# Kernel optimization log

Measured on AMD Instinct MI355X. Metric: run time of the kernel, lower is better.

## Reference

```python
import jax, jax.numpy as jnp
import numpy as np
from jax import lax

HIDDEN = 7168
Q_LORA = 1536
N_HEAD = 64
HEAD_DIM = 128
ROPE_DIM = 64
TOPK = 2048
T = 4096
ROPE_BASE = 10000.0
LN_EPS = 1e-6
NEG_INF = -1e30


def _apply_rope_interleaved(x, cos, sin):
    # x: [..., ROPE_DIM], cos/sin broadcastable to [..., ROPE_DIM//2]
    x1 = x[..., 0::2]
    x2 = x[..., 1::2]
    o1 = x1 * cos - x2 * sin
    o2 = x1 * sin + x2 * cos
    out = jnp.stack([o1, o2], axis=-1)  # interleave back
    return out.reshape(x.shape)


def setup_inputs() -> dict:
    key = jax.random.key(0)
    ks = jax.random.split(key, 6)
    hidden_states = jax.random.normal(ks[0], (T, HIDDEN), dtype=jnp.float32)
    qr = jax.random.normal(ks[1], (T, Q_LORA), dtype=jnp.float32)
    positions = jnp.arange(T, dtype=jnp.int32)
    # learned parameters (stored [in, out] so fwd is x @ W)
    Wq_b = jax.random.normal(ks[2], (Q_LORA, N_HEAD * HEAD_DIM), dtype=jnp.float32) * 0.02
    Wk = jax.random.normal(ks[3], (HIDDEN, HEAD_DIM), dtype=jnp.float32) * 0.02
    Wproj = jax.random.normal(ks[4], (HIDDEN, N_HEAD), dtype=jnp.float32) * 0.02
    k_norm_gamma = jnp.ones((HEAD_DIM,), dtype=jnp.float32)
    k_norm_beta = jnp.zeros((HEAD_DIM,), dtype=jnp.float32)
    return {
        'hidden_states': hidden_states,
        'qr': qr,
        'positions': positions,
        'Wq_b': Wq_b,
        'Wk': Wk,
        'Wproj': Wproj,
        'k_norm_gamma': k_norm_gamma,
        'k_norm_beta': k_norm_beta,
    }


def _indexer_forward(hidden_states, qr, positions, Wq_b, Wk, Wproj, gamma, beta):
    # q projection: [T, n_head * head_dim] -> [T, H, D]
    q = (qr @ Wq_b).reshape(T, N_HEAD, HEAD_DIM)
    q_pe, q_nope = q[..., :ROPE_DIM], q[..., ROPE_DIM:]

    # k projection + LayerNorm (eps=1e-6)
    k = hidden_states @ Wk  # [T, D]
    mu = jnp.mean(k, axis=-1, keepdims=True)
    var = jnp.mean(jnp.square(k - mu), axis=-1, keepdims=True)
    k = (k - mu) * lax.rsqrt(var + LN_EPS) * gamma + beta
    k_pe, k_nope = k[..., :ROPE_DIM], k[..., ROPE_DIM:]

    # RoPE (interleaved / GPT-J style, as used by DeepSeek rotary)
    inv_freq = 1.0 / (ROPE_BASE ** (jnp.arange(0, ROPE_DIM, 2, dtype=jnp.float32) / ROPE_DIM))
    ang = positions.astype(jnp.float32)[:, None] * inv_freq[None, :]  # [T, R/2]
    cos, sin = jnp.cos(ang), jnp.sin(ang)
    q_pe = _apply_rope_interleaved(q_pe, cos[:, None, :], sin[:, None, :])  # [T, H, R]
    k_pe = _apply_rope_interleaved(k_pe, cos, sin)  # [T, R]

    q_full = jnp.concatenate([q_pe, q_nope], axis=-1)  # [T, H, D]
    k_full = jnp.concatenate([k_pe, k_nope], axis=-1)  # [T, D]

    # per-token per-head weights, scaled by head_dim**-0.5 * n_head**-0.5
    w = (hidden_states @ Wproj) * (HEAD_DIM ** -0.5) * (N_HEAD ** -0.5)  # [T, H]

    # lightning-indexer score: sum_h w[t,h] * relu(q[t,h,:] . k[s,:])
    # scan over heads so live intermediate is a single [T, T] matrix
    qh_all = jnp.transpose(q_full, (1, 0, 2))  # [H, T, D]
    wh_all = w.T  # [H, T]

    def body(acc, hw):
        qh, wh = hw  # [T, D], [T]
        acc = acc + wh[:, None] * jax.nn.relu(qh @ k_full.T)
        return acc, None

    scores, _ = lax.scan(body, jnp.zeros((T, T), dtype=jnp.float32), (qh_all, wh_all))

    # causal mask over key positions, then select top-k keys per query
    causal = positions[:, None] >= positions[None, :]
    masked = jnp.where(causal, scores, NEG_INF)
    topk_vals, topk_idx = lax.top_k(masked, TOPK)  # [T, TOPK]
    return topk_vals, topk_idx


def reference(hidden_states, qr, positions, Wq_b, Wk, Wproj, k_norm_gamma, k_norm_beta):
    return _indexer_forward(hidden_states, qr, positions, Wq_b, Wk, Wproj, k_norm_gamma, k_norm_beta)
```

## Files before the change

### kernel.cpp

```cpp
#include <hip/hip_runtime.h>
#include <stdint.h>

#define TT 4096
#define HID 7168
#define QL 1536
#define NH 64
#define HD 128
#define QD 8192
#define KTOP 2048
#define WSCALE 0.011048543456039806f

typedef _Float16 f16;
typedef uint16_t u16;
typedef unsigned u32;
typedef __attribute__((ext_vector_type(4))) float f32x4;
typedef __attribute__((ext_vector_type(16))) float f32x16;
typedef __attribute__((ext_vector_type(8))) _Float16 f16x8;
typedef __attribute__((ext_vector_type(4))) _Float16 f16x4;

__device__ __forceinline__ void lds_load16(const void* g, void* l) {
  __builtin_amdgcn_global_load_lds(
      (const __attribute__((address_space(1))) unsigned*)g,
      (__attribute__((address_space(3))) unsigned*)l, 16, 0, 0);
}

__device__ __forceinline__ u16 f16_bits(f16 h) {
  union { f16 h; u16 u; } c; c.h = h; return c.u;
}
__device__ __forceinline__ float f16_from_bits(u16 u) {
  union { u16 u; f16 h; } c; c.u = u; return (float)c.h;
}

__device__ __forceinline__ size_t soff(int t) {
  int b = t >> 7, r = t & 127;
  return (size_t)128u * ((size_t)(b + 1) * (size_t)(64 * b + r));
}

__global__ void tcvt(const float* __restrict__ in, f16* __restrict__ out,
                     int R, int C, int ostride, int orow0) {
  __shared__ float tile[32][33];
  int cb = blockIdx.x * 32, rb = blockIdx.y * 32;
  int tx = threadIdx.x & 31, ty = threadIdx.x >> 5;
  for (int i = 0; i < 32; i += 8)
    tile[ty + i][tx] = in[(size_t)(rb + ty + i) * C + cb + tx];
  __syncthreads();
  for (int i = 0; i < 32; i += 8)
    out[(size_t)(cb + ty + i + orow0) * ostride + rb + tx] = (f16)tile[tx][ty + i];
}

__launch_bounds__(256, 2)
__global__ void gemm_q(const float* __restrict__ A, const f16* __restrict__ B, f16* __restrict__ C) {
  __shared__ __align__(16) f16 As[128 * 32];
  __shared__ __align__(16) f16 Bs[128 * 32];
  int tid = threadIdx.x, lane = tid & 63, wave = tid >> 6;
  int bm = blockIdx.y << 7, bn = blockIdx.x << 7;
  int wm = (wave & 1) << 6, wn = (wave >> 1) << 6;
  const f16* gb = B + (size_t)(bn + (tid >> 2)) * QL + (tid & 3) * 8;
  f16* lB = Bs + wave * 512;
  int ar = tid >> 3, ac = (tid & 7) * 4;
  f32x4 acc[4][4] = {};
  for (int k0 = 0; k0 < QL; k0 += 32) {
    __syncthreads();
#pragma unroll
    for (int i = 0; i < 4; i++) {
      float4 v = *(const float4*)(A + (size_t)(bm + ar + i * 32) * QL + k0 + ac);
      f16x4 h = {(f16)v.x, (f16)v.y, (f16)v.z, (f16)v.w};
      *(f16x4*)(As + (ar + i * 32) * 32 + ac) = h;
    }
    lds_load16(gb + k0, lB);
    lds_load16(gb + (size_t)64 * QL + k0, lB + 2048);
    __syncthreads();
    int ro = lane & 15, ko = (lane >> 4) << 3;
    f16x8 af[4], bf[4];
#pragma unroll
    for (int i = 0; i < 4; i++) af[i] = *(const f16x8*)(As + (wm + i * 16 + ro) * 32 + ko);
#pragma unroll
    for (int i = 0; i < 4; i++) bf[i] = *(const f16x8*)(Bs + (wn + i * 16 + ro) * 32 + ko);
#pragma unroll
    for (int mi = 0; mi < 4; mi++)
#pragma unroll
      for (int ni = 0; ni < 4; ni++)
        acc[mi][ni] = __builtin_amdgcn_mfma_f32_16x16x32_f16(af[mi], bf[ni], acc[mi][ni], 0, 0, 0);
  }
  int cr = (lane >> 4) << 2, cc = lane & 15;
#pragma unroll
  for (int mi = 0; mi < 4; mi++)
#pragma unroll
    for (int ni = 0; ni < 4; ni++) {
      int row = bm + wm + mi * 16 + cr;
      int col = bn + wn + ni * 16 + cc;
      f16* cp = C + (size_t)row * QD + col;
#pragma unroll
      for (int r = 0; r < 4; r++) cp[(size_t)r * QD] = (f16)acc[mi][ni][r];
    }
}

__launch_bounds__(256, 2)
__global__ void gemm_kw(const float* __restrict__ A, const f16* __restrict__ B,
                        float* __restrict__ kraw, float* __restrict__ wout) {
  __shared__ __align__(16) f16 As[64 * 64];
  __shared__ __align__(16) f16 Bs[64 * 64];
  int tid = threadIdx.x, lane = tid & 63, wave = tid >> 6;
  int bm = blockIdx.y << 6, bn = blockIdx.x << 6;
  int wm = (wave & 1) << 5, wn = (wave >> 1) << 5;
  const f16* gb = B + (size_t)(bn + (tid >> 3)) * HID + (tid & 7) * 8;
  f16* lB = Bs + wave * 512;
  int ar = tid >> 4, ac = (tid & 15) * 4;
  f32x4 acc[2][2] = {};
  for (int k0 = 0; k0 < HID; k0 += 64) {
    __syncthreads();
#pragma unroll
    for (int i = 0; i < 4; i++) {
      float4 v = *(const float4*)(A + (size_t)(bm + ar + i * 16) * HID + k0 + ac);
      f16x4 h = {(f16)v.x, (f16)v.y, (f16)v.z, (f16)v.w};
      *(f16x4*)(As + (ar + i * 16) * 64 + ac) = h;
    }
    lds_load16(gb + k0, lB);
    lds_load16(gb + (size_t)32 * HID + k0, lB + 2048);
    __syncthreads();
    int ro = lane & 15, ko = (lane >> 4) << 3;
    f16x8 af[2][2], bf[2][2];
#pragma unroll
    for (int i = 0; i < 2; i++)
#pragma unroll
      for (int kk = 0; kk < 2; kk++) {
        af[i][kk] = *(const f16x8*)(As + (wm + i * 16 + ro) * 64 + kk * 32 + ko);
        bf[i][kk] = *(const f16x8*)(Bs + (wn + i * 16 + ro) * 64 + kk * 32 + ko);
      }
#pragma unroll
    for (int mi = 0; mi < 2; mi++)
#pragma unroll
      for (int ni = 0; ni < 2; ni++)
#pragma unroll
        for (int kk = 0; kk < 2; kk++)
          acc[mi][ni] = __builtin_amdgcn_mfma_f32_16x16x32_f16(af[mi][kk], bf[ni][kk], acc[mi][ni], 0, 0, 0);
  }
  int cr = (lane >> 4) << 2, cc = lane & 15;
#pragma unroll
  for (int mi = 0; mi < 2; mi++)
#pragma unroll
    for (int ni = 0; ni < 2; ni++) {
      int row = bm + wm + mi * 16 + cr;
      int col = bn + wn + ni * 16 + cc;
#pragma unroll
      for (int r = 0; r < 4; r++) {
        float v = acc[mi][ni][r];
        int rr = row + r;
        if (col < HD) kraw[(size_t)rr * HD + col] = v;
        else          wout[(size_t)rr * NH + (col - HD)] = v * WSCALE;
      }
    }
}

__global__ void ln_rope(const float* __restrict__ kraw, const int* __restrict__ pos,
                        const float* __restrict__ gamma, const float* __restrict__ beta,
                        f16* __restrict__ k16) {
  int row = (blockIdx.x << 2) + (threadIdx.x >> 6);
  int lane = threadIdx.x & 63;
  const float* kr = kraw + (size_t)row * HD;
  float2 x = ((const float2*)kr)[lane];
  float s = x.x + x.y, s2 = x.x * x.x + x.y * x.y;
  for (int off = 32; off; off >>= 1) { s += __shfl_down(s, off); s2 += __shfl_down(s2, off); }
  s = __shfl(s, 0); s2 = __shfl(s2, 0);
  float mu = s * (1.f / 128.f);
  float var = s2 * (1.f / 128.f) - mu * mu;
  float inv = rsqrtf(var + 1e-6f);
  float y0 = (x.x - mu) * inv * gamma[lane * 2] + beta[lane * 2];
  float y1 = (x.y - mu) * inv * gamma[lane * 2 + 1] + beta[lane * 2 + 1];
  float o0 = y0, o1 = y1;
  if (lane < 32) {
    float p = (float)pos[row];
    float invf = exp2f(-(float)lane * 0.41524101185942813f);
    float ang = p * invf;
    float sn, cn;
    sincosf(ang, &sn, &cn);
    o0 = y0 * cn - y1 * sn;
    o1 = y0 * sn + y1 * cn;
  }
  k16[(size_t)row * HD + 2 * lane] = (f16)o0;
  k16[(size_t)row * HD + 2 * lane + 1] = (f16)o1;
}

__global__ void rope_q(f16* __restrict__ q16, const int* __restrict__ pos) {
  int t = blockIdx.x, tid = threadIdx.x;
  __shared__ float cs[64];
  if (tid < 32) {
    float invf = exp2f(-(float)tid * 0.41524101185942813f);
    float ang = (float)pos[t] * invf;
    float sn, cn;
    sincosf(ang, &sn, &cn);
    cs[tid] = cn;
    cs[32 + tid] = sn;
  }
  __syncthreads();
  f16* row = q16 + (size_t)t * QD;
#pragma unroll
  for (int it = 0; it < 2; it++) {
    int u = it * 256 + tid;
    int h = u >> 3, c = u & 7;
    f16* p = row + h * HD + c * 8;
    f16x8 v = *(f16x8*)p;
#pragma unroll
    for (int j = 0; j < 4; j++) {
      int l = c * 4 + j;
      float cn = cs[l], sn = cs[32 + l];
      float x = (float)v[2 * j], y = (float)v[2 * j + 1];
      v[2 * j] = (f16)(x * cn - y * sn);
      v[2 * j + 1] = (f16)(x * sn + y * cn);
    }
    *(f16x8*)p = v;
  }
}

__launch_bounds__(256, 3)
__global__ void scores2(const f16* __restrict__ q16, const f16* __restrict__ k16,
                        const float* __restrict__ w, f16* __restrict__ S) {
  int kt0 = blockIdx.x << 8;
  int qt0 = blockIdx.y << 5;
  if (kt0 > qt0 + 31) return;
  int tid = threadIdx.x, l = tid & 63, wid = tid >> 6;
  int q = l & 31, half = l >> 5;
  __shared__ __align__(16) f16 smem_q[8192];
  __shared__ float w_lds[2048];

  for (int i = tid; i < 2048; i += 256) {
    int hh = i & 63, qq = i >> 6;
    w_lds[hh * 32 + qq] = w[(size_t)(qt0 + qq) * NH + hh];
  }
  f16x8 kfr[2][8];
  {
    const f16* kb = k16 + (size_t)(kt0 + wid * 64 + q) * HD + half * 8;
#pragma unroll
    for (int mt = 0; mt < 2; mt++)
#pragma unroll
      for (int kk = 0; kk < 8; kk++)
        kfr[mt][kk] = *(const f16x8*)(kb + mt * 32 * HD + kk * 16);
  }
  const f16* qbase = q16 + (size_t)qt0 * QD;
#pragma unroll
  for (int p = 0; p < 2; p++) {
    int u = p * 256 + tid;
    lds_load16(qbase + (size_t)(u & 31) * QD + (u >> 5) * 8, smem_q + u * 8);
  }
  f32x16 s0 = {}, s1 = {};
  __syncthreads();

  for (int h = 0; h < NH; h++) {
    if (h < NH - 1) {
      const f16* src = qbase + (h + 1) * HD;
      f16* dst = smem_q + ((h + 1) & 1) * 4096;
#pragma unroll
      for (int p = 0; p < 2; p++) {
        int u = p * 256 + tid;
        lds_load16(src + (size_t)(u & 31) * QD + (u >> 5) * 8, dst + u * 8);
      }
    }
    const f16* qb = smem_q + (h & 1) * 4096;
    f32x16 a0 = {}, a1 = {};
#pragma unroll
    for (int kk = 0; kk < 8; kk++) {
      f16x8 qf = *(const f16x8*)(qb + ((kk * 2 + half) * 32 + q) * 8);
      a0 = __builtin_amdgcn_mfma_f32_32x32x16_f16(kfr[0][kk], qf, a0, 0, 0, 0);
      a1 = __builtin_amdgcn_mfma_f32_32x32x16_f16(kfr[1][kk], qf, a1, 0, 0, 0);
    }
    float wv = w_lds[h * 32 + q];
#pragma unroll
    for (int r = 0; r < 16; r++) {
      s0[r] += wv * fmaxf(a0[r], 0.f);
      s1[r] += wv * fmaxf(a1[r], 0.f);
    }
    __syncthreads();
  }

  f16* st = smem_q;
#pragma unroll
  for (int mt = 0; mt < 2; mt++)
#pragma unroll
    for (int r = 0; r < 16; r++) {
      int m = (r & 3) + ((r >> 2) << 3) + half * 4;
      int sl = wid * 64 + mt * 32 + m;
      float v = mt ? s1[r] : s0[r];
      if (!(v == v)) v = 0.f;
      v = fminf(fmaxf(v, -60000.f), 60000.f);
      u32 byte = (u32)(q * 512 + sl * 2) ^ (u32)((q & 7) << 4);
      *(f16*)((char*)st + byte) = (f16)v;
    }
  __syncthreads();
  {
    int rq = tid >> 3, c = tid & 7;
    int t = qt0 + rq;
    size_t base = soff(t) + (size_t)kt0;
    bool hi = (t - kt0) >= 128;
#pragma unroll
    for (int j = 0; j < 4; j++) {
      if (c < 4 || hi) {
        u32 byte = (u32)(rq * 512 + c * 64 + j * 16) ^ (u32)((rq & 7) << 4);
        uint4 v = *(uint4*)((char*)st + byte);
        *(uint4*)(S + base + c * 32 + j * 8) = v;
      }
    }
  }
}

template <int N>
__device__ __forceinline__ void sort_and_store(u32* key, int tid, int t, float* out) {
  constexpr int V = N / 256;
  u32 v[V];
#pragma unroll
  for (int r = 0; r < V; r += 4) {
    uint4 q4 = *(const uint4*)(key + tid * V + r);
    v[r] = ~q4.x; v[r + 1] = ~q4.y; v[r + 2] = ~q4.z; v[r + 3] = ~q4.w;
  }
#pragma unroll
  for (int k = 2; k <= N; k <<= 1) {
#pragma unroll
    for (int j = k >> 1; j > 0; j >>= 1) {
      if (j >= 64 * V) {
#pragma unroll
        for (int r = 0; r < V; r += 4) {
          uint4 q4 = {v[r], v[r + 1], v[r + 2], v[r + 3]};
          *(uint4*)(key + tid * V + r) = q4;
        }
        __syncthreads();
        for (int m = tid; m < N / 2; m += 256) {
          int i = ((m & ~(j - 1)) << 1) | (m & (j - 1));
          int l = i | j;
          bool up = ((i & k) == 0);
          u32 a = key[i], b = key[l];
          if (up ? (a > b) : (a < b)) { key[i] = b; key[l] = a; }
        }
        __syncthreads();
#pragma unroll
        for (int r = 0; r < V; r += 4) {
          uint4 q4 = *(const uint4*)(key + tid * V + r);
          v[r] = q4.x; v[r + 1] = q4.y; v[r + 2] = q4.z; v[r + 3] = q4.w;
        }
      } else if (j >= V) {
        int lanej = j / V;
        bool takeMin = (((tid & lanej) == 0) == (((tid * V) & k) == 0));
#pragma unroll
        for (int r = 0; r < V; r++) {
          u32 o = __shfl_xor(v[r], lanej, 64);
          u32 mn = min(v[r], o), mx = max(v[r], o);
          v[r] = takeMin ? mn : mx;
        }
      } else {
#pragma unroll
        for (int r = 0; r < V; r++) {
          if ((r & j) == 0) {
            bool up = (((tid * V + r) & k) == 0);
            u32 a = v[r], b = v[r | j];
            u32 mn = min(a, b), mx = max(a, b);
            v[r] = up ? mn : mx;
            v[r | j] = up ? mx : mn;
          }
        }
      }
    }
  }
  if (tid * V < KTOP) {
    float* ov = out + (size_t)t * KTOP + tid * V;
    float* oi = out + (size_t)TT * KTOP + (size_t)t * KTOP + tid * V;
#pragma unroll
    for (int r = 0; r < V; r++) {
      u32 kv = ~v[r];
      u32 mono = kv >> 16;
      float val;
      if (mono == 0u) {
        val = -1e30f;
      } else {
        u16 hb = (u16)((mono & 0x8000u) ? (mono ^ 0x8000u) : (mono ^ 0xFFFFu));
        val = f16_from_bits(hb);
      }
      ov[r] = val;
      oi[r] = (float)(0xFFFFu - (kv & 0xFFFFu));
    }
  }
}

__launch_bounds__(256, 4)
__global__ void topk_k(const f16* __restrict__ S, float* __restrict__ out) {
  int t = blockIdx.x, tid = threadIdx.x;
  __shared__ __align__(16) u32 key[4096];
  size_t base = soff(t);
  int nsort = (t <= 2047) ? 2048 : 4096;
  const uint4* src = (const uint4*)(S + base);
  for (int i = tid; i < (nsort >> 3); i += 256) {
    uint4 v4 = src[i];
    u32 ww[4] = {v4.x, v4.y, v4.z, v4.w};
#pragma unroll
    for (int j = 0; j < 8; j++) {
      int s = i * 8 + j;
      u32 kk;
      if (s > t) {
        kk = 0xFFFFu - (u32)s;
      } else {
        u16 hb = (u16)(ww[j >> 1] >> ((j & 1) * 16));
        u32 mono = (hb & 0x8000u) ? (u32)(hb ^ 0xFFFFu) : (u32)(hb | 0x8000u);
        kk = (mono << 16) | (0xFFFFu - (u32)s);
      }
      key[s] = kk;
    }
  }
  __syncthreads();
  if (t <= 2047) sort_and_store<2048>(key, tid, t, out);
  else           sort_and_store<4096>(key, tid, t, out);
}

extern "C" void kernel_launch(void* const* d_in, const int* in_sizes, int n_in,
                              void* d_out, int out_size, void* d_ws, size_t ws_size,
                              hipStream_t stream) {
  const float* hs = (const float*)d_in[0];
  const float* qr = (const float*)d_in[1];
  const int* pos = (const int*)d_in[2];
  const float* Wq = (const float*)d_in[3];
  const float* Wk = (const float*)d_in[4];
  const float* Wp = (const float*)d_in[5];
  const float* gamma = (const float*)d_in[6];
  const float* beta = (const float*)d_in[7];
  char* ws = (char*)d_ws;
  float* kraw = (float*)ws;
  float* wsc = (float*)(ws + 2097152);
  f16* k16 = (f16*)(ws + 3145728);
  f16* kwT = (f16*)(ws + 4194304);
  f16* wqT = (f16*)(ws + 6946816);
  f16* q16 = (f16*)(ws + 32112640);
  f16* S = (f16*)(ws + 4194304);

  tcvt<<<dim3(256, 48), dim3(256), 0, stream>>>(Wq, wqT, QL, QD, QL, 0);
  tcvt<<<dim3(4, 224), dim3(256), 0, stream>>>(Wk, kwT, HID, HD, HID, 0);
  tcvt<<<dim3(2, 224), dim3(256), 0, stream>>>(Wp, kwT, HID, NH, HID, HD);
  gemm_kw<<<dim3(3, 64), dim3(256), 0, stream>>>(hs, kwT, kraw, wsc);
  ln_rope<<<dim3(1024), dim3(256), 0, stream>>>(kraw, pos, gamma, beta, k16);
  gemm_q<<<dim3(64, 32), dim3(256), 0, stream>>>(qr, wqT, q16);
  rope_q<<<dim3(4096), dim3(256), 0, stream>>>(q16, pos);
  scores2<<<dim3(16, 128), dim3(256), 0, stream>>>(q16, k16, wsc, S);
  topk_k<<<dim3(4096), dim3(256), 0, stream>>>(S, (float*)d_out);
}
```

Before: 860.1 us.

## Launch only causal score tiles and deepen Q staging to four-stage pipeline

Replaces the 16x128 grid with early-exit blocks by a compact 1088-block grid that maps each block to a lower-triangular (query, key) tile, interleaved across XCDs. The per-head Q staging in shared memory goes from double to quad buffering, with explicit vmcnt waits and raw barriers so three heads are in flight, and MFMA sections get raised wave priority. This is meant to remove the cost of empty blocks, hide global-to-LDS latency, and cut full __syncthreads overhead. In exchange LDS use doubles, which may lower occupancy, and the hand-written waitcnt counts must match the number of outstanding loads.

```diff
diff --git a/kernel.cpp b/kernel.cpp
--- a/kernel.cpp
+++ b/kernel.cpp
@@ -215,12 +215,18 @@
 __launch_bounds__(256, 3)
 __global__ void scores2(const f16* __restrict__ q16, const f16* __restrict__ k16,
                         const float* __restrict__ w, f16* __restrict__ S) {
-  int kt0 = blockIdx.x << 8;
-  int qt0 = blockIdx.y << 5;
-  if (kt0 > qt0 + 31) return;
+  int bid = (int)blockIdx.x;
+  bid = (bid & 7) * 136 + (bid >> 3);
+  int g = 0;
+  while (4 * (g + 1) * (g + 2) <= bid) g++;
+  int rem = bid - 4 * g * (g + 1);
+  int qt = (g << 3) + rem / (g + 1);
+  int kt = rem - (rem / (g + 1)) * (g + 1);
+  int kt0 = kt << 8, qt0 = qt << 5;
+
   int tid = threadIdx.x, l = tid & 63, wid = tid >> 6;
   int q = l & 31, half = l >> 5;
-  __shared__ __align__(16) f16 smem_q[8192];
+  __shared__ __align__(16) f16 smem_q[4 * 4096];
   __shared__ float w_lds[2048];
 
   for (int i = tid; i < 2048; i += 256) {
@@ -236,41 +242,60 @@
       for (int kk = 0; kk < 8; kk++)
         kfr[mt][kk] = *(const f16x8*)(kb + mt * 32 * HD + kk * 16);
   }
+  __syncthreads();
+  asm volatile("s_waitcnt vmcnt(0)" ::: "memory");
+
   const f16* qbase = q16 + (size_t)qt0 * QD;
-#pragma unroll
-  for (int p = 0; p < 2; p++) {
-    int u = p * 256 + tid;
-    lds_load16(qbase + (size_t)(u & 31) * QD + (u >> 5) * 8, smem_q + u * 8);
-  }
+  auto stage = [&](int h) {
+    const f16* src = qbase + h * HD;
+    f16* dst = smem_q + (h & 3) * 4096;
+#pragma unroll
+    for (int p = 0; p < 2; p++) {
+      int u = p * 256 + tid;
+      lds_load16(src + (size_t)(u & 31) * QD + (u >> 5) * 8, dst + u * 8);
+    }
+  };
+
   f32x16 s0 = {}, s1 = {};
-  __syncthreads();
-
-  for (int h = 0; h < NH; h++) {
-    if (h < NH - 1) {
-      const f16* src = qbase + (h + 1) * HD;
-      f16* dst = smem_q + ((h + 1) & 1) * 4096;
-#pragma unroll
-      for (int p = 0; p < 2; p++) {
-        int u = p * 256 + tid;
-        lds_load16(src + (size_t)(u & 31) * QD + (u >> 5) * 8, dst + u * 8);
-      }
-    }
-    const f16* qb = smem_q + (h & 1) * 4096;
+  auto compute = [&](int h) {
+    const f16* qb = smem_q + (h & 3) * 4096;
     f32x16 a0 = {}, a1 = {};
+    __builtin_amdgcn_s_setprio(1);
 #pragma unroll
     for (int kk = 0; kk < 8; kk++) {
       f16x8 qf = *(const f16x8*)(qb + ((kk * 2 + half) * 32 + q) * 8);
       a0 = __builtin_amdgcn_mfma_f32_32x32x16_f16(kfr[0][kk], qf, a0, 0, 0, 0);
       a1 = __builtin_amdgcn_mfma_f32_32x32x16_f16(kfr[1][kk], qf, a1, 0, 0, 0);
     }
+    __builtin_amdgcn_s_setprio(0);
     float wv = w_lds[h * 32 + q];
 #pragma unroll
     for (int r = 0; r < 16; r++) {
       s0[r] += wv * fmaxf(a0[r], 0.f);
       s1[r] += wv * fmaxf(a1[r], 0.f);
     }
-    __syncthreads();
-  }
+  };
+
+  stage(0); stage(1); stage(2);
+  for (int h = 0; h < 61; h++) {
+    asm volatile("s_waitcnt vmcnt(4)" ::: "memory");
+    __builtin_amdgcn_s_barrier();
+    asm volatile("" ::: "memory");
+    stage(h + 3);
+    compute(h);
+  }
+  asm volatile("s_waitcnt vmcnt(4)" ::: "memory");
+  __builtin_amdgcn_s_barrier();
+  asm volatile("" ::: "memory");
+  compute(61);
+  asm volatile("s_waitcnt vmcnt(2)" ::: "memory");
+  __builtin_amdgcn_s_barrier();
+  asm volatile("" ::: "memory");
+  compute(62);
+  asm volatile("s_waitcnt vmcnt(0)" ::: "memory");
+  __builtin_amdgcn_s_barrier();
+  asm volatile("" ::: "memory");
+  compute(63);
 
   f16* st = smem_q;
 #pragma unroll
@@ -434,6 +459,6 @@
   ln_rope<<<dim3(1024), dim3(256), 0, stream>>>(kraw, pos, gamma, beta, k16);
   gemm_q<<<dim3(64, 32), dim3(256), 0, stream>>>(qr, wqT, q16);
   rope_q<<<dim3(4096), dim3(256), 0, stream>>>(q16, pos);
-  scores2<<<dim3(16, 128), dim3(256), 0, stream>>>(q16, k16, wsc, S);
+  scores2<<<dim3(1088), dim3(256), 0, stream>>>(q16, k16, wsc, S);
   topk_k<<<dim3(4096), dim3(256), 0, stream>>>(S, (float*)d_out);
 }
```

Result: faster. 813.5 us (-5.4%).

## Load Q fragments into registers directly and launch only causal score tiles

Applied to the files above, without the earlier changes.

The scores kernel now loads each head's Q fragment straight from global memory into registers, double-buffered across head pairs, instead of staging it through LDS. This removes the per-head __syncthreads. The grid becomes a compact 1D launch of only the causal (q-tile, k-tile) pairs, with a swizzled block order, so no blocks start and exit early. MFMA sections get raised wave priority. The cost is more VGPRs, so occupancy drops from 3 to 2 blocks, and there are redundant global reads of Q across waves.

```diff
diff --git a/kernel.cpp b/kernel.cpp
--- a/kernel.cpp
+++ b/kernel.cpp
@@ -212,16 +212,22 @@
   }
 }
 
-__launch_bounds__(256, 3)
-__global__ void scores2(const f16* __restrict__ q16, const f16* __restrict__ k16,
+__launch_bounds__(256, 2)
+__global__ void scores4(const f16* __restrict__ q16, const f16* __restrict__ k16,
                         const float* __restrict__ w, f16* __restrict__ S) {
-  int kt0 = blockIdx.x << 8;
-  int qt0 = blockIdx.y << 5;
-  if (kt0 > qt0 + 31) return;
+  int bid = (int)blockIdx.x;
+  bid = (bid & 7) * 136 + (bid >> 3);
+  int g = 0;
+  while (4 * (g + 1) * (g + 2) <= bid) g++;
+  int rem = bid - 4 * g * (g + 1);
+  int qt = (g << 3) + rem / (g + 1);
+  int kt = rem - (rem / (g + 1)) * (g + 1);
+  int kt0 = kt << 8, qt0 = qt << 5;
+
   int tid = threadIdx.x, l = tid & 63, wid = tid >> 6;
   int q = l & 31, half = l >> 5;
-  __shared__ __align__(16) f16 smem_q[8192];
-  __shared__ float w_lds[2048];
+  __shared__ __align__(16) unsigned char smem[16384];
+  float* w_lds = (float*)smem;
 
   for (int i = tid; i < 2048; i += 256) {
     int hh = i & 63, qq = i >> 6;
@@ -236,43 +242,46 @@
       for (int kk = 0; kk < 8; kk++)
         kfr[mt][kk] = *(const f16x8*)(kb + mt * 32 * HD + kk * 16);
   }
-  const f16* qbase = q16 + (size_t)qt0 * QD;
-#pragma unroll
-  for (int p = 0; p < 2; p++) {
-    int u = p * 256 + tid;
-    lds_load16(qbase + (size_t)(u & 31) * QD + (u >> 5) * 8, smem_q + u * 8);
-  }
+  __syncthreads();
+
+  const f16* qrow = q16 + (size_t)(qt0 + q) * QD + half * 8;
+  f16x8 qa[8], qb[8];
+#pragma unroll
+  for (int kk = 0; kk < 8; kk++) qa[kk] = *(const f16x8*)(qrow + kk * 16);
+
   f32x16 s0 = {}, s1 = {};
-  __syncthreads();
-
-  for (int h = 0; h < NH; h++) {
-    if (h < NH - 1) {
-      const f16* src = qbase + (h + 1) * HD;
-      f16* dst = smem_q + ((h + 1) & 1) * 4096;
-#pragma unroll
-      for (int p = 0; p < 2; p++) {
-        int u = p * 256 + tid;
-        lds_load16(src + (size_t)(u & 31) * QD + (u >> 5) * 8, dst + u * 8);
-      }
-    }
-    const f16* qb = smem_q + (h & 1) * 4096;
+  auto compute = [&](const f16x8 (&qf)[8], int h) {
+    float wv = w_lds[h * 32 + q];
     f32x16 a0 = {}, a1 = {};
+    __builtin_amdgcn_s_setprio(1);
 #pragma unroll
     for (int kk = 0; kk < 8; kk++) {
-      f16x8 qf = *(const f16x8*)(qb + ((kk * 2 + half) * 32 + q) * 8);
-      a0 = __builtin_amdgcn_mfma_f32_32x32x16_f16(kfr[0][kk], qf, a0, 0, 0, 0);
-      a1 = __builtin_amdgcn_mfma_f32_32x32x16_f16(kfr[1][kk], qf, a1, 0, 0, 0);
-    }
-    float wv = w_lds[h * 32 + q];
+      a0 = __builtin_amdgcn_mfma_f32_32x32x16_f16(kfr[0][kk], qf[kk], a0, 0, 0, 0);
+      a1 = __builtin_amdgcn_mfma_f32_32x32x16_f16(kfr[1][kk], qf[kk], a1, 0, 0, 0);
+    }
+    __builtin_amdgcn_s_setprio(0);
 #pragma unroll
     for (int r = 0; r < 16; r++) {
       s0[r] += wv * fmaxf(a0[r], 0.f);
       s1[r] += wv * fmaxf(a1[r], 0.f);
     }
-    __syncthreads();
-  }
-
-  f16* st = smem_q;
+  };
+
+  for (int h = 0; h < NH; h += 2) {
+    const f16* src1 = qrow + (size_t)(h + 1) * HD;
+#pragma unroll
+    for (int kk = 0; kk < 8; kk++) qb[kk] = *(const f16x8*)(src1 + kk * 16);
+    compute(qa, h);
+    if (h + 2 < NH) {
+      const f16* src2 = qrow + (size_t)(h + 2) * HD;
+#pragma unroll
+      for (int kk = 0; kk < 8; kk++) qa[kk] = *(const f16x8*)(src2 + kk * 16);
+    }
+    compute(qb, h + 1);
+  }
+  __syncthreads();
+
+  f16* st = (f16*)smem;
 #pragma unroll
   for (int mt = 0; mt < 2; mt++)
 #pragma unroll
@@ -434,6 +443,6 @@
   ln_rope<<<dim3(1024), dim3(256), 0, stream>>>(kraw, pos, gamma, beta, k16);
   gemm_q<<<dim3(64, 32), dim3(256), 0, stream>>>(qr, wqT, q16);
   rope_q<<<dim3(4096), dim3(256), 0, stream>>>(q16, pos);
-  scores2<<<dim3(16, 128), dim3(256), 0, stream>>>(q16, k16, wsc, S);
+  scores4<<<dim3(1088), dim3(256), 0, stream>>>(q16, k16, wsc, S);
   topk_k<<<dim3(4096), dim3(256), 0, stream>>>(S, (float*)d_out);
 }
```

New measurement: 911.7 us. 6.0% more time.
